# Performance work log

Measured on AMD Instinct MI355X. Metric: run time of the kernel, lower is better.

Reference implementation:

```python
import jax, jax.numpy as jnp
import numpy as np

N_EMBD = 1024
N_HEAD = 16
HEAD = N_EMBD // N_HEAD  # 64
N_HIDDEN = 2816          # ((int(2*4*1024/3)-1)//256)*256 + 256
BLOCK_SIZE = 4096
EPS = 1e-5


def rope_cos_sin(T, hd, base=10000.0):
    theta = 1.0 / (base ** (jnp.arange(0, hd, 2, dtype=jnp.float32) / hd))  # (hd/2,)
    idx = jnp.arange(T, dtype=jnp.float32)
    ang = jnp.outer(idx, theta)  # (T, hd/2)
    return jnp.cos(ang), jnp.sin(ang)


def apply_rope(x, cos, sin):
    # x: (B, H, T, hd); rotate interleaved pairs (x0,x1),(x2,x3),...
    xp = x.reshape(*x.shape[:-1], HEAD // 2, 2)
    xe, xo = xp[..., 0], xp[..., 1]
    c = cos[None, None, :, :]
    s = sin[None, None, :, :]
    oe = xe * c - xo * s
    oo = xe * s + xo * c
    return jnp.stack([oe, oo], axis=-1).reshape(x.shape)


def rmsnorm(x, scale):
    ms = jnp.mean(x * x, axis=-1, keepdims=True)
    return scale * (x * jax.lax.rsqrt(ms + EPS))


def setup_inputs() -> dict:
    key = jax.random.key(0)
    ks = jax.random.split(key, 9)
    B, T = 2, 2048
    x = jax.random.normal(ks[0], (B, T, N_EMBD), dtype=jnp.float32)
    y_mask = jax.random.randint(ks[1], (B, 64), 0, 2, dtype=jnp.int32)
    sd = 1.0 / np.sqrt(N_EMBD)
    Wqkv = jax.random.normal(ks[2], (N_EMBD, 3 * N_EMBD), dtype=jnp.float32) * sd
    Wattn_proj = jax.random.normal(ks[3], (N_EMBD, N_EMBD), dtype=jnp.float32) * sd
    scale1 = jnp.ones((N_EMBD,), dtype=jnp.float32)
    scale2 = jnp.ones((N_EMBD,), dtype=jnp.float32)
    Wfc1 = jax.random.normal(ks[4], (N_EMBD, N_HIDDEN), dtype=jnp.float32) * sd
    Wfc2 = jax.random.normal(ks[5], (N_EMBD, N_HIDDEN), dtype=jnp.float32) * sd
    Wmlp_proj = jax.random.normal(ks[6], (N_HIDDEN, N_EMBD), dtype=jnp.float32) / np.sqrt(N_HIDDEN)
    return {"x": x, "y_mask": y_mask, "Wqkv": Wqkv, "Wattn_proj": Wattn_proj,
            "scale1": scale1, "scale2": scale2, "Wfc1": Wfc1, "Wfc2": Wfc2,
            "Wmlp_proj": Wmlp_proj}


def reference(x, y_mask, Wqkv, Wattn_proj, scale1, scale2, Wfc1, Wfc2, Wmlp_proj):
    B, T, C = x.shape
    # ---- attention branch (pre-RMSNorm) ----
    h = rmsnorm(x, scale1)
    qkv = h @ Wqkv  # (B, T, 3C)
    q, k, v = jnp.split(qkv, 3, axis=-1)
    q = q.reshape(B, T, N_HEAD, HEAD).transpose(0, 2, 1, 3)
    k = k.reshape(B, T, N_HEAD, HEAD).transpose(0, 2, 1, 3)
    v = v.reshape(B, T, N_HEAD, HEAD).transpose(0, 2, 1, 3)
    cos, sin = rope_cos_sin(T, HEAD)
    q = apply_rope(q, cos, sin)
    k = apply_rope(k, cos, sin)
    # mixed causal + text-text bidirectional mask
    causal = jnp.tril(jnp.ones((T, T), dtype=bool))  # (T, T)
    ym = y_mask.astype(bool)  # (B, L)
    L = ym.shape[1]
    text = ym[:, :, None] & ym[:, None, :]  # (B, L, L)
    text = jnp.pad(text, ((0, 0), (0, T - L), (0, T - L)))
    mask = jnp.logical_or(causal[None, :, :], text)  # (B, T, T)
    scale = 1.0 / np.sqrt(HEAD)
    scores = jnp.einsum('bhqd,bhkd->bhqk', q, k) * scale
    scores = jnp.where(mask[:, None, :, :], scores, -jnp.inf)
    attn = jax.nn.softmax(scores, axis=-1)
    y = jnp.einsum('bhqk,bhkd->bhqd', attn, v)
    y = y.transpose(0, 2, 1, 3).reshape(B, T, C)
    x = x + y @ Wattn_proj
    # ---- SwiGLU MLP branch (pre-RMSNorm) ----
    h2 = rmsnorm(x, scale2)
    m = jax.nn.silu(h2 @ Wfc1) * (h2 @ Wfc2)
    x = x + m @ Wmlp_proj
    return x
```

## Files before the change

### kernel.cpp

```cpp
#include <hip/hip_runtime.h>
#include <stdint.h>

typedef unsigned short u16;
typedef __attribute__((ext_vector_type(8))) short bf16x8;
typedef __attribute__((ext_vector_type(4))) float f32x4;

__device__ __forceinline__ float b2f(u16 u) {
    union { float f; uint32_t u; } v; v.u = ((uint32_t)u) << 16; return v.f;
}
__device__ __forceinline__ u16 f2b(float f) {
    union { float f; uint32_t u; } v; v.f = f;
    uint32_t r = v.u + 0x7FFFu + ((v.u >> 16) & 1u);
    return (u16)(r >> 16);
}
__device__ __forceinline__ uint32_t cvt_pk_bf16(float lo, float hi) {
    uint32_t r;
    asm("v_cvt_pk_bf16_f32 %0, %1, %2" : "=v"(r) : "v"(lo), "v"(hi));
    return r;
}

template <int CTRL>
__device__ __forceinline__ float dppf(float x) {
    union { float f; int i; } u; u.f = x;
    u.i = __builtin_amdgcn_update_dpp(0, u.i, CTRL, 0xF, 0xF, false);
    return u.f;
}
__device__ __forceinline__ float rowmax16(float v) {
    v = fmaxf(v, dppf<0x121>(v));
    v = fmaxf(v, dppf<0x122>(v));
    v = fmaxf(v, dppf<0x124>(v));
    v = fmaxf(v, dppf<0x128>(v));
    return v;
}
__device__ __forceinline__ float rowsum16(float v) {
    v += dppf<0x121>(v);
    v += dppf<0x122>(v);
    v += dppf<0x124>(v);
    v += dppf<0x128>(v);
    return v;
}

__device__ __forceinline__ void stage16(const void* g, void* l) {
    __builtin_amdgcn_global_load_lds(
        (const __attribute__((address_space(1))) uint32_t*)(uintptr_t)g,
        (__attribute__((address_space(3))) uint32_t*)(uint32_t)(uintptr_t)l,
        16, 0, 0);
}

__global__ __launch_bounds__(256) void prep_kernel(const float* __restrict__ Wqkv,
                                                   const float* __restrict__ Wattn,
                                                   const float* __restrict__ Wfc1,
                                                   const float* __restrict__ Wfc2,
                                                   const float* __restrict__ Wmlp,
                                                   u16* WtQ, u16* WtA, u16* WtF1,
                                                   u16* WtF2, u16* WtM,
                                                   const float* __restrict__ xin,
                                                   const float* __restrict__ scale,
                                                   u16* __restrict__ xout) {
    const int tx = threadIdx.x, ty = threadIdx.y;
    int id = blockIdx.x;
    if (id >= 12544) {
        const int row = id - 12544, tid = ty * 32 + tx;
        const float4 v = ((const float4*)(xin + (size_t)row * 1024))[tid];
        float ss = v.x * v.x + v.y * v.y + v.z * v.z + v.w * v.w;
        #pragma unroll
        for (int d = 32; d; d >>= 1) ss += __shfl_xor(ss, d);
        __shared__ float wsum[4];
        if ((tid & 63) == 0) wsum[tid >> 6] = ss;
        __syncthreads();
        const float r = rsqrtf((wsum[0] + wsum[1] + wsum[2] + wsum[3]) * (1.f / 1024.f) + 1e-5f);
        const float4 sc = ((const float4*)scale)[tid];
        uint2 o;
        o.x = cvt_pk_bf16(v.x * sc.x * r, v.y * sc.y * r);
        o.y = cvt_pk_bf16(v.z * sc.z * r, v.w * sc.w * r);
        ((uint2*)(xout + (size_t)row * 1024))[tid] = o;
        return;
    }
    __shared__ u16 tile[32][33];
    const float* src; u16* dst; int R, C;
    if (id < 3072)      {             src = Wqkv;  dst = WtQ;  R = 1024; C = 3072; }
    else if (id < 4096) { id -= 3072; src = Wattn; dst = WtA;  R = 1024; C = 1024; }
    else if (id < 6912) { id -= 4096; src = Wfc1;  dst = WtF1; R = 1024; C = 2816; }
    else if (id < 9728) { id -= 6912; src = Wfc2;  dst = WtF2; R = 1024; C = 2816; }
    else                { id -= 9728; src = Wmlp;  dst = WtM;  R = 2816; C = 1024; }
    const int nbx = C >> 5;
    const int bx = id % nbx, by = id / nbx;
    const int cx = bx * 32, ry = by * 32;
    #pragma unroll
    for (int i = 0; i < 32; i += 8)
        tile[ty + i][tx] = f2b(src[(size_t)(ry + ty + i) * C + cx + tx]);
    __syncthreads();
    #pragma unroll
    for (int i = 0; i < 32; i += 8)
        dst[(size_t)(cx + ty + i) * R + ry + tx] = tile[tx][ty + i];
}

__global__ __launch_bounds__(256) void rmsnorm_f32(const float* __restrict__ xin,
                                                   const float* __restrict__ scale,
                                                   u16* __restrict__ out) {
    const int row = blockIdx.x, tid = threadIdx.x;
    const float4 v = ((const float4*)(xin + (size_t)row * 1024))[tid];
    float ss = v.x * v.x + v.y * v.y + v.z * v.z + v.w * v.w;
    #pragma unroll
    for (int d = 32; d; d >>= 1) ss += __shfl_xor(ss, d);
    __shared__ float wsum[4];
    if ((tid & 63) == 0) wsum[tid >> 6] = ss;
    __syncthreads();
    const float r = rsqrtf((wsum[0] + wsum[1] + wsum[2] + wsum[3]) * (1.f / 1024.f) + 1e-5f);
    const float4 sc = ((const float4*)scale)[tid];
    uint2 o;
    o.x = cvt_pk_bf16(v.x * sc.x * r, v.y * sc.y * r);
    o.y = cvt_pk_bf16(v.z * sc.z * r, v.w * sc.w * r);
    ((uint2*)(out + (size_t)row * 1024))[tid] = o;
}

__global__ __launch_bounds__(256) void rope_kernel(u16* __restrict__ qkv) {
    const int gid = blockIdx.x * 256 + threadIdx.x;
    const int i = gid & 31;
    const int row = gid >> 5;
    const int tpos = row & 2047;
    const float theta = expf(-(float)i * (9.210340371976184f / 32.0f));
    const float ang = (float)tpos * theta;
    const float c = cosf(ang), s = sinf(ang);
    uint32_t* p = (uint32_t*)qkv + (size_t)row * 1536 + i;
    #pragma unroll
    for (int h = 0; h < 16; ++h) {
        const uint32_t uq = p[h * 32];
        {
            const float xe = b2f((u16)(uq & 0xffff)), xo = b2f((u16)(uq >> 16));
            p[h * 32] = cvt_pk_bf16(xe * c - xo * s, xe * s + xo * c);
        }
        const uint32_t uk = p[512 + h * 32];
        {
            const float xe = b2f((u16)(uk & 0xffff)), xo = b2f((u16)(uk >> 16));
            p[512 + h * 32] = cvt_pk_bf16(xe * c - xo * s, xe * s + xo * c);
        }
    }
}

template <int EPI>
__global__ __launch_bounds__(256) void gemm_bt(const u16* __restrict__ A,
                                               const u16* __restrict__ Bt,
                                               void* __restrict__ Cout,
                                               const void* __restrict__ Res,
                                               int N, int K) {
    __shared__ __attribute__((aligned(16))) u16 As[2][128 * 32];
    __shared__ __attribute__((aligned(16))) u16 Bs[2][128 * 32];
    const int tid = threadIdx.x;
    const int w = tid >> 6, lane = tid & 63;
    const int quad = lane >> 4, t = lane & 15;
    const int m0 = blockIdx.y * 128, n0 = blockIdx.x * 128;
    const int wm = (w >> 1) * 64, wn = (w & 1) * 64;

    const int srow = w * 16 + (lane >> 2);
    const int scol = (lane & 3) * 8;
    const u16* pA0 = A + (size_t)(m0 + srow) * K + scol;
    const u16* pA1 = pA0 + (size_t)64 * K;
    const u16* pB0 = Bt + (size_t)(n0 + srow) * K + scol;
    const u16* pB1 = pB0 + (size_t)64 * K;

    f32x4 acc[4][4];
    #pragma unroll
    for (int i = 0; i < 4; ++i)
        #pragma unroll
        for (int j = 0; j < 4; ++j) acc[i][j] = (f32x4){0.f, 0.f, 0.f, 0.f};

    for (int kb = 0; kb < K; kb += 64) {
        __syncthreads();
        stage16(pA0 + kb,      (char*)As[0] + w * 1024);
        stage16(pA1 + kb,      (char*)As[0] + 4096 + w * 1024);
        stage16(pB0 + kb,      (char*)Bs[0] + w * 1024);
        stage16(pB1 + kb,      (char*)Bs[0] + 4096 + w * 1024);
        stage16(pA0 + kb + 32, (char*)As[1] + w * 1024);
        stage16(pA1 + kb + 32, (char*)As[1] + 4096 + w * 1024);
        stage16(pB0 + kb + 32, (char*)Bs[1] + w * 1024);
        stage16(pB1 + kb + 32, (char*)Bs[1] + 4096 + w * 1024);
        __syncthreads();
        #pragma unroll
        for (int hf = 0; hf < 2; ++hf) {
            bf16x8 af[4], bfr[4];
            #pragma unroll
            for (int mi = 0; mi < 4; ++mi)
                af[mi] = *(const bf16x8*)((char*)As[hf] + (wm + mi * 16 + t) * 64 + quad * 16);
            #pragma unroll
            for (int ni = 0; ni < 4; ++ni)
                bfr[ni] = *(const bf16x8*)((char*)Bs[hf] + (wn + ni * 16 + t) * 64 + quad * 16);
            #pragma unroll
            for (int mi = 0; mi < 4; ++mi)
                #pragma unroll
                for (int ni = 0; ni < 4; ++ni)
                    acc[mi][ni] = __builtin_amdgcn_mfma_f32_16x16x32_bf16(af[mi], bfr[ni],
                                                                         acc[mi][ni], 0, 0, 0);
        }
    }
    #pragma unroll
    for (int mi = 0; mi < 4; ++mi) {
        const int row0 = m0 + wm + mi * 16 + quad * 4;
        #pragma unroll
        for (int ni = 0; ni < 4; ++ni) {
            const int col = n0 + wn + ni * 16 + t;
            #pragma unroll
            for (int r = 0; r < 4; r += 2) {
                const size_t idx0 = (size_t)(row0 + r) * N + col;
                const size_t idx1 = (size_t)(row0 + r + 1) * N + col;
                if (EPI == 0) {
                    const uint32_t pk2 = cvt_pk_bf16(acc[mi][ni][r], acc[mi][ni][r + 1]);
                    ((u16*)Cout)[idx0] = (u16)pk2;
                    ((u16*)Cout)[idx1] = (u16)(pk2 >> 16);
                } else {
                    ((float*)Cout)[idx0] = acc[mi][ni][r]     + ((const float*)Res)[idx0];
                    ((float*)Cout)[idx1] = acc[mi][ni][r + 1] + ((const float*)Res)[idx1];
                }
            }
        }
    }
}

template <int EPI>
__global__ __launch_bounds__(256) void gemm_bt64(const u16* __restrict__ A,
                                                 const u16* __restrict__ Bt,
                                                 void* __restrict__ Cout,
                                                 const float* __restrict__ Res,
                                                 int N, int K) {
    __shared__ __attribute__((aligned(16))) u16 As[2][128 * 32];
    __shared__ __attribute__((aligned(16))) u16 Bs[2][64 * 32];
    const int tid = threadIdx.x;
    const int w = tid >> 6, lane = tid & 63;
    const int quad = lane >> 4, t = lane & 15;
    const int m0 = blockIdx.y * 128, n0 = blockIdx.x * 64;
    const int wm = (w >> 1) * 64, wn = (w & 1) * 32;

    const int srow = w * 16 + (lane >> 2);
    const int scol = (lane & 3) * 8;
    const u16* pA0 = A + (size_t)(m0 + srow) * K + scol;
    const u16* pA1 = pA0 + (size_t)64 * K;
    const u16* pB0 = Bt + (size_t)(n0 + srow) * K + scol;

    f32x4 acc[4][2];
    #pragma unroll
    for (int i = 0; i < 4; ++i)
        #pragma unroll
        for (int j = 0; j < 2; ++j) acc[i][j] = (f32x4){0.f, 0.f, 0.f, 0.f};

    for (int kb = 0; kb < K; kb += 64) {
        __syncthreads();
        stage16(pA0 + kb,      (char*)As[0] + w * 1024);
        stage16(pA1 + kb,      (char*)As[0] + 4096 + w * 1024);
        stage16(pB0 + kb,      (char*)Bs[0] + w * 1024);
        stage16(pA0 + kb + 32, (char*)As[1] + w * 1024);
        stage16(pA1 + kb + 32, (char*)As[1] + 4096 + w * 1024);
        stage16(pB0 + kb + 32, (char*)Bs[1] + w * 1024);
        __syncthreads();
        #pragma unroll
        for (int hf = 0; hf < 2; ++hf) {
            bf16x8 af[4], bfr[2];
            #pragma unroll
            for (int mi = 0; mi < 4; ++mi)
                af[mi] = *(const bf16x8*)((char*)As[hf] + (wm + mi * 16 + t) * 64 + quad * 16);
            #pragma unroll
            for (int ni = 0; ni < 2; ++ni)
                bfr[ni] = *(const bf16x8*)((char*)Bs[hf] + (wn + ni * 16 + t) * 64 + quad * 16);
            #pragma unroll
            for (int mi = 0; mi < 4; ++mi)
                #pragma unroll
                for (int ni = 0; ni < 2; ++ni)
                    acc[mi][ni] = __builtin_amdgcn_mfma_f32_16x16x32_bf16(af[mi], bfr[ni],
                                                                         acc[mi][ni], 0, 0, 0);
        }
    }
    #pragma unroll
    for (int mi = 0; mi < 4; ++mi) {
        const int row0 = m0 + wm + mi * 16 + quad * 4;
        #pragma unroll
        for (int ni = 0; ni < 2; ++ni) {
            const int col = n0 + wn + ni * 16 + t;
            #pragma unroll
            for (int r = 0; r < 4; ++r) {
                const size_t idx = (size_t)(row0 + r) * N + col;
                const float v = acc[mi][ni][r];
                if (EPI == 0) ((u16*)Cout)[idx]   = f2b(v);
                else          ((float*)Cout)[idx] = v + Res[idx];
            }
        }
    }
}

__global__ __launch_bounds__(256) void gemm_fc(const u16* __restrict__ A,
                                               const u16* __restrict__ B1t,
                                               const u16* __restrict__ B2t,
                                               u16* __restrict__ Cout,
                                               int N, int K) {
    __shared__ __attribute__((aligned(16))) u16 As[2][128 * 32];
    __shared__ __attribute__((aligned(16))) u16 B1s[2][64 * 32];
    __shared__ __attribute__((aligned(16))) u16 B2s[2][64 * 32];
    const int tid = threadIdx.x;
    const int w = tid >> 6, lane = tid & 63;
    const int quad = lane >> 4, t = lane & 15;
    const int m0 = blockIdx.y * 128, n0 = blockIdx.x * 64;
    const int wm = (w >> 1) * 64, wn = (w & 1) * 32;

    const int srow = w * 16 + (lane >> 2);
    const int scol = (lane & 3) * 8;
    const u16* pA0 = A + (size_t)(m0 + srow) * K + scol;
    const u16* pA1 = pA0 + (size_t)64 * K;
    const u16* pB1 = B1t + (size_t)(n0 + srow) * K + scol;
    const u16* pB2 = B2t + (size_t)(n0 + srow) * K + scol;

    f32x4 acc1[4][2], acc2[4][2];
    #pragma unroll
    for (int i = 0; i < 4; ++i)
        #pragma unroll
        for (int j = 0; j < 2; ++j) {
            acc1[i][j] = (f32x4){0.f, 0.f, 0.f, 0.f};
            acc2[i][j] = (f32x4){0.f, 0.f, 0.f, 0.f};
        }

    for (int kb = 0; kb < K; kb += 64) {
        __syncthreads();
        stage16(pA0 + kb,      (char*)As[0] + w * 1024);
        stage16(pA1 + kb,      (char*)As[0] + 4096 + w * 1024);
        stage16(pB1 + kb,      (char*)B1s[0] + w * 1024);
        stage16(pB2 + kb,      (char*)B2s[0] + w * 1024);
        stage16(pA0 + kb + 32, (char*)As[1] + w * 1024);
        stage16(pA1 + kb + 32, (char*)As[1] + 4096 + w * 1024);
        stage16(pB1 + kb + 32, (char*)B1s[1] + w * 1024);
        stage16(pB2 + kb + 32, (char*)B2s[1] + w * 1024);
        __syncthreads();
        #pragma unroll
        for (int hf = 0; hf < 2; ++hf) {
            bf16x8 af[4], b1r[2], b2r[2];
            #pragma unroll
            for (int mi = 0; mi < 4; ++mi)
                af[mi] = *(const bf16x8*)((char*)As[hf] + (wm + mi * 16 + t) * 64 + quad * 16);
            #pragma unroll
            for (int ni = 0; ni < 2; ++ni) {
                b1r[ni] = *(const bf16x8*)((char*)B1s[hf] + (wn + ni * 16 + t) * 64 + quad * 16);
                b2r[ni] = *(const bf16x8*)((char*)B2s[hf] + (wn + ni * 16 + t) * 64 + quad * 16);
            }
            #pragma unroll
            for (int mi = 0; mi < 4; ++mi)
                #pragma unroll
                for (int ni = 0; ni < 2; ++ni) {
                    acc1[mi][ni] = __builtin_amdgcn_mfma_f32_16x16x32_bf16(af[mi], b1r[ni],
                                                                          acc1[mi][ni], 0, 0, 0);
                    acc2[mi][ni] = __builtin_amdgcn_mfma_f32_16x16x32_bf16(af[mi], b2r[ni],
                                                                          acc2[mi][ni], 0, 0, 0);
                }
        }
    }
    #pragma unroll
    for (int mi = 0; mi < 4; ++mi) {
        const int row0 = m0 + wm + mi * 16 + quad * 4;
        #pragma unroll
        for (int ni = 0; ni < 2; ++ni) {
            const int col = n0 + wn + ni * 16 + t;
            float mv[4];
            #pragma unroll
            for (int r = 0; r < 4; ++r) {
                const float a = acc1[mi][ni][r];
                mv[r] = (a / (1.f + __expf(-a))) * acc2[mi][ni][r];
            }
            #pragma unroll
            for (int r = 0; r < 4; r += 2) {
                const uint32_t pk2 = cvt_pk_bf16(mv[r], mv[r + 1]);
                Cout[(size_t)(row0 + r) * N + col]     = (u16)pk2;
                Cout[(size_t)(row0 + r + 1) * N + col] = (u16)(pk2 >> 16);
            }
        }
    }
}

__global__ __launch_bounds__(256) void attn_kernel(const u16* __restrict__ qkv,
                                                   const int* __restrict__ ymask,
                                                   u16* __restrict__ y) {
    const int gid = blockIdx.x;
    const int xcd = gid & 7;
    const int j2 = gid >> 3;
    const int slot = j2 >> 4;
    const int pairk = j2 & 15;
    const int group = slot * 8 + xcd;
    const int h = group & 15, b = group >> 4;
    const int tid = threadIdx.x;
    const int w = tid >> 6, lane = tid & 63;
    const int quad = lane >> 4, t = lane & 15;

    __shared__ __attribute__((aligned(16))) u16 Ks[64 * 72];
    __shared__ __attribute__((aligned(16))) u16 Vts[64 * 72];
    __shared__ __attribute__((aligned(16))) u16 Ps[4][16 * 72];
    __shared__ int ymL[64];
    if (pairk == 0 && tid < 64) ymL[tid] = ymask[b * 64 + tid];

    const int skey = tid >> 3, sdg = tid & 7;
    const u16* pK = qkv + (size_t)(b * 2048 + skey) * 3072 + h * 64 + sdg * 8 + 1024;
    const int sblk0 = (skey >> 3) ^ sdg;
    const int sblk1 = (4 + (skey >> 3)) ^ sdg;

    for (int seg = 0; seg < 2; ++seg) {
        const int qt = seg ? pairk : 31 - pairk;
        const int q0 = qt * 64;

        bf16x8 aQ[2];
        {
            const u16* qp = qkv + (size_t)(b * 2048 + q0 + w * 16 + t) * 3072 + h * 64 + quad * 8;
            aQ[0] = *(const bf16x8*)qp;
            aQ[1] = *(const bf16x8*)(qp + 32);
            #pragma unroll
            for (int i = 0; i < 8; ++i) {
                aQ[0][i] = (short)f2b(b2f((u16)aQ[0][i]) * 0.125f);
                aQ[1][i] = (short)f2b(b2f((u16)aQ[1][i]) * 0.125f);
            }
        }

        f32x4 accO[4] = {(f32x4){0,0,0,0},(f32x4){0,0,0,0},(f32x4){0,0,0,0},(f32x4){0,0,0,0}};
        float mOld[4] = {-INFINITY, -INFINITY, -INFINITY, -INFINITY};
        float lSum[4] = {0.f, 0.f, 0.f, 0.f};

        for (int kb = 0; kb <= qt; ++kb) {
            const u16* pk = pK + (size_t)kb * 196608;
            const uint4 kv0 = *(const uint4*)pk;
            const uint4 vv0 = *(const uint4*)(pk + 1024);
            const uint4 kv1 = *(const uint4*)(pk + 98304);
            const uint4 vv1 = *(const uint4*)(pk + 99328);
            __syncthreads();
            *(uint4*)((char*)Ks + skey * 144 + sdg * 16) = kv0;
            *(uint4*)((char*)Ks + (skey + 32) * 144 + sdg * 16) = kv1;
            {
                const u16* vp0 = (const u16*)&vv0;
                const u16* vp1 = (const u16*)&vv1;
                #pragma unroll
                for (int jj = 0; jj < 8; ++jj) {
                    const int row = sdg * 8 + jj;
                    Vts[row * 72 + sblk0 * 8 + (skey & 7)] = vp0[jj];
                    Vts[row * 72 + sblk1 * 8 + (skey & 7)] = vp1[jj];
                }
            }
            __syncthreads();

            float s[4][4];
            __builtin_amdgcn_s_setprio(1);
            #pragma unroll
            for (int ni = 0; ni < 4; ++ni) {
                bf16x8 bK0 = *(const bf16x8*)((char*)Ks + (ni * 16 + t) * 144 + quad * 16);
                bf16x8 bK1 = *(const bf16x8*)((char*)Ks + (ni * 16 + t) * 144 + 64 + quad * 16);
                f32x4 sa = (f32x4){0.f, 0.f, 0.f, 0.f};
                sa = __builtin_amdgcn_mfma_f32_16x16x32_bf16(aQ[0], bK0, sa, 0, 0, 0);
                sa = __builtin_amdgcn_mfma_f32_16x16x32_bf16(aQ[1], bK1, sa, 0, 0, 0);
                #pragma unroll
                for (int r = 0; r < 4; ++r) s[ni][r] = sa[r];
            }
            __builtin_amdgcn_s_setprio(0);

            if (kb == qt) {
                const int irow = q0 + w * 16 + quad * 4;
                #pragma unroll
                for (int ni = 0; ni < 4; ++ni)
                    #pragma unroll
                    for (int r = 0; r < 4; ++r) {
                        const int i = irow + r, j = kb * 64 + ni * 16 + t;
                        const bool ok = (j <= i) || (qt == 0 && ymL[i & 63] && ymL[j & 63]);
                        if (!ok) s[ni][r] = -INFINITY;
                    }
            }

            float alpha[4];
            bool upd = false;
            #pragma unroll
            for (int r = 0; r < 4; ++r) {
                float mt = fmaxf(fmaxf(s[0][r], s[1][r]), fmaxf(s[2][r], s[3][r]));
                mt = rowmax16(mt);
                const float mNew = fmaxf(mOld[r], mt);
                upd = upd || (mNew > mOld[r]);
                alpha[r] = __expf(mOld[r] - mNew);
                #pragma unroll
                for (int ni = 0; ni < 4; ++ni) s[ni][r] = __expf(s[ni][r] - mNew);
                mOld[r] = mNew;
            }

            u16* Pw = Ps[w];
            #pragma unroll
            for (int ni = 0; ni < 4; ++ni)
                #pragma unroll
                for (int r = 0; r < 4; ++r)
                    Pw[(quad * 4 + r) * 72 + ni * 16 + t] = f2b(s[ni][r]);

            #pragma unroll
            for (int r = 0; r < 4; ++r) {
                float rs = (s[0][r] + s[1][r]) + (s[2][r] + s[3][r]);
                rs = rowsum16(rs);
                lSum[r] = lSum[r] * alpha[r] + rs;
            }
            if (__any(upd)) {
                #pragma unroll
                for (int dt = 0; dt < 4; ++dt)
                    #pragma unroll
                    for (int r = 0; r < 4; ++r) accO[dt][r] *= alpha[r];
            }

            bf16x8 aP0 = *(const bf16x8*)((char*)Pw + t * 144 + quad * 16);
            bf16x8 aP1 = *(const bf16x8*)((char*)Pw + t * 144 + 64 + quad * 16);
            __builtin_amdgcn_s_setprio(1);
            #pragma unroll
            for (int dt = 0; dt < 4; ++dt) {
                const int row = dt * 16 + t, rb = row >> 3;
                bf16x8 bV0 = *(const bf16x8*)((char*)Vts + row * 144 + ((quad ^ rb) << 4));
                bf16x8 bV1 = *(const bf16x8*)((char*)Vts + row * 144 + (((4 + quad) ^ rb) << 4));
                accO[dt] = __builtin_amdgcn_mfma_f32_16x16x32_bf16(aP0, bV0, accO[dt], 0, 0, 0);
                accO[dt] = __builtin_amdgcn_mfma_f32_16x16x32_bf16(aP1, bV1, accO[dt], 0, 0, 0);
            }
            __builtin_amdgcn_s_setprio(0);
        }
        const int orow = q0 + w * 16 + quad * 4;
        #pragma unroll
        for (int dt = 0; dt < 4; ++dt)
            #pragma unroll
            for (int r = 0; r < 4; ++r) {
                const size_t idx = (size_t)(b * 2048 + orow + r) * 1024 + h * 64 + dt * 16 + t;
                y[idx] = f2b(accO[dt][r] / lSum[r]);
            }
    }
}

extern "C" void kernel_launch(void* const* d_in, const int* in_sizes, int n_in,
                              void* d_out, int out_size, void* d_ws, size_t ws_size,
                              hipStream_t stream) {
    const float* x     = (const float*)d_in[0];
    const int*   ym    = (const int*)d_in[1];
    const float* Wqkv  = (const float*)d_in[2];
    const float* Wattn = (const float*)d_in[3];
    const float* s1    = (const float*)d_in[4];
    const float* s2    = (const float*)d_in[5];
    const float* Wfc1  = (const float*)d_in[6];
    const float* Wfc2  = (const float*)d_in[7];
    const float* Wmlp  = (const float*)d_in[8];

    char* ws = (char*)d_ws;
    u16*    h    = (u16*)(ws + 0);
    u16*    qkv  = (u16*)(ws + 8388608);
    u16*    fc1  = qkv;
    float*  xr   = (float*)(ws + 33554432);
    u16*    WtA  = (u16*)(ws + 50331648);
    u16*    WtF1 = (u16*)(ws + 52428800);
    u16*    WtF2 = (u16*)(ws + 58195968);
    u16*    WtM  = (u16*)(ws + 63963136);
    u16*    WtQ  = (u16*)(ws + 73400320);
    const dim3 tb(32, 8);

    prep_kernel<<<16640, tb, 0, stream>>>(Wqkv, Wattn, Wfc1, Wfc2, Wmlp,
                                          WtQ, WtA, WtF1, WtF2, WtM, x, s1, h);
    gemm_bt<0><<<dim3(24, 32), 256, 0, stream>>>(h, WtQ, qkv, nullptr, 3072, 1024);
    rope_kernel<<<512, 256, 0, stream>>>(qkv);
    attn_kernel<<<512, 256, 0, stream>>>(qkv, ym, h);
    gemm_bt64<1><<<dim3(16, 32), 256, 0, stream>>>(h, WtA, xr, x, 1024, 1024);
    rmsnorm_f32<<<4096, 256, 0, stream>>>(xr, s2, h);
    gemm_fc<<<dim3(44, 32), 256, 0, stream>>>(h, WtF1, WtF2, fc1, 2816, 1024);
    gemm_bt64<1><<<dim3(16, 32), 256, 0, stream>>>(fc1, WtM, (float*)d_out, xr, 1024, 2816);
}
```

Baseline: 347.8 us.

## Double-buffer K/V tiles in attention kernel with register prefetch

K and V shared-memory tiles become double-buffered. The next key block's global loads are issued into registers before the current block's QK and PV MFMAs, then written to the alternate buffer afterward. This cuts the loop from two barriers to one per iteration and hides global load latency behind compute. It doubles K/V LDS usage, which may reduce occupancy, and adds register pressure from the prefetched values.

New measurement: 347.8 us. No clear change (-0.0%).

```diff
diff --git a/kernel.cpp b/kernel.cpp
--- a/kernel.cpp
+++ b/kernel.cpp
@@ -384,8 +384,8 @@
     const int w = tid >> 6, lane = tid & 63;
     const int quad = lane >> 4, t = lane & 15;
 
-    __shared__ __attribute__((aligned(16))) u16 Ks[64 * 72];
-    __shared__ __attribute__((aligned(16))) u16 Vts[64 * 72];
+    __shared__ __attribute__((aligned(16))) u16 Ks[2][64 * 72];
+    __shared__ __attribute__((aligned(16))) u16 Vts[2][64 * 72];
     __shared__ __attribute__((aligned(16))) u16 Ps[4][16 * 72];
     __shared__ int ymL[64];
     if (pairk == 0 && tid < 64) ymL[tid] = ymask[b * 64 + tid];
@@ -411,37 +411,49 @@
             }
         }
 
+        {
+            const uint4 kv0 = *(const uint4*)pK;
+            const uint4 vv0 = *(const uint4*)(pK + 1024);
+            const uint4 kv1 = *(const uint4*)(pK + 98304);
+            const uint4 vv1 = *(const uint4*)(pK + 99328);
+            __syncthreads();
+            *(uint4*)((char*)Ks[0] + skey * 144 + sdg * 16) = kv0;
+            *(uint4*)((char*)Ks[0] + (skey + 32) * 144 + sdg * 16) = kv1;
+            const u16* vp0 = (const u16*)&vv0;
+            const u16* vp1 = (const u16*)&vv1;
+            #pragma unroll
+            for (int jj = 0; jj < 8; ++jj) {
+                const int row = sdg * 8 + jj;
+                Vts[0][row * 72 + sblk0 * 8 + (skey & 7)] = vp0[jj];
+                Vts[0][row * 72 + sblk1 * 8 + (skey & 7)] = vp1[jj];
+            }
+        }
+        __syncthreads();
+
         f32x4 accO[4] = {(f32x4){0,0,0,0},(f32x4){0,0,0,0},(f32x4){0,0,0,0},(f32x4){0,0,0,0}};
         float mOld[4] = {-INFINITY, -INFINITY, -INFINITY, -INFINITY};
         float lSum[4] = {0.f, 0.f, 0.f, 0.f};
 
+        int cur = 0;
         for (int kb = 0; kb <= qt; ++kb) {
-            const u16* pk = pK + (size_t)kb * 196608;
-            const uint4 kv0 = *(const uint4*)pk;
-            const uint4 vv0 = *(const uint4*)(pk + 1024);
-            const uint4 kv1 = *(const uint4*)(pk + 98304);
-            const uint4 vv1 = *(const uint4*)(pk + 99328);
-            __syncthreads();
-            *(uint4*)((char*)Ks + skey * 144 + sdg * 16) = kv0;
-            *(uint4*)((char*)Ks + (skey + 32) * 144 + sdg * 16) = kv1;
-            {
-                const u16* vp0 = (const u16*)&vv0;
-                const u16* vp1 = (const u16*)&vv1;
-                #pragma unroll
-                for (int jj = 0; jj < 8; ++jj) {
-                    const int row = sdg * 8 + jj;
-                    Vts[row * 72 + sblk0 * 8 + (skey & 7)] = vp0[jj];
-                    Vts[row * 72 + sblk1 * 8 + (skey & 7)] = vp1[jj];
-                }
-            }
-            __syncthreads();
+            const bool more = (kb < qt);
+            uint4 nk0, nv0, nk1, nv1;
+            if (more) {
+                const u16* pk = pK + (size_t)(kb + 1) * 196608;
+                nk0 = *(const uint4*)pk;
+                nv0 = *(const uint4*)(pk + 1024);
+                nk1 = *(const uint4*)(pk + 98304);
+                nv1 = *(const uint4*)(pk + 99328);
+            }
+            const u16* KsC  = Ks[cur];
+            const u16* VtsC = Vts[cur];
 
             float s[4][4];
             __builtin_amdgcn_s_setprio(1);
             #pragma unroll
             for (int ni = 0; ni < 4; ++ni) {
-                bf16x8 bK0 = *(const bf16x8*)((char*)Ks + (ni * 16 + t) * 144 + quad * 16);
-                bf16x8 bK1 = *(const bf16x8*)((char*)Ks + (ni * 16 + t) * 144 + 64 + quad * 16);
+                bf16x8 bK0 = *(const bf16x8*)((const char*)KsC + (ni * 16 + t) * 144 + quad * 16);
+                bf16x8 bK1 = *(const bf16x8*)((const char*)KsC + (ni * 16 + t) * 144 + 64 + quad * 16);
                 f32x4 sa = (f32x4){0.f, 0.f, 0.f, 0.f};
                 sa = __builtin_amdgcn_mfma_f32_16x16x32_bf16(aQ[0], bK0, sa, 0, 0, 0);
                 sa = __builtin_amdgcn_mfma_f32_16x16x32_bf16(aQ[1], bK1, sa, 0, 0, 0);
@@ -502,12 +514,30 @@
             #pragma unroll
             for (int dt = 0; dt < 4; ++dt) {
                 const int row = dt * 16 + t, rb = row >> 3;
-                bf16x8 bV0 = *(const bf16x8*)((char*)Vts + row * 144 + ((quad ^ rb) << 4));
-                bf16x8 bV1 = *(const bf16x8*)((char*)Vts + row * 144 + (((4 + quad) ^ rb) << 4));
+                bf16x8 bV0 = *(const bf16x8*)((const char*)VtsC + row * 144 + ((quad ^ rb) << 4));
+                bf16x8 bV1 = *(const bf16x8*)((const char*)VtsC + row * 144 + (((4 + quad) ^ rb) << 4));
                 accO[dt] = __builtin_amdgcn_mfma_f32_16x16x32_bf16(aP0, bV0, accO[dt], 0, 0, 0);
                 accO[dt] = __builtin_amdgcn_mfma_f32_16x16x32_bf16(aP1, bV1, accO[dt], 0, 0, 0);
             }
             __builtin_amdgcn_s_setprio(0);
+
+            if (!more) break;
+            {
+                u16* KsN  = Ks[cur ^ 1];
+                u16* VtsN = Vts[cur ^ 1];
+                *(uint4*)((char*)KsN + skey * 144 + sdg * 16) = nk0;
+                *(uint4*)((char*)KsN + (skey + 32) * 144 + sdg * 16) = nk1;
+                const u16* vp0 = (const u16*)&nv0;
+                const u16* vp1 = (const u16*)&nv1;
+                #pragma unroll
+                for (int jj = 0; jj < 8; ++jj) {
+                    const int row = sdg * 8 + jj;
+                    VtsN[row * 72 + sblk0 * 8 + (skey & 7)] = vp0[jj];
+                    VtsN[row * 72 + sblk1 * 8 + (skey & 7)] = vp1[jj];
+                }
+            }
+            __syncthreads();
+            cur ^= 1;
         }
         const int orow = q0 + w * 16 + quad * 4;
         #pragma unroll
```
